# Optimization experiments

Hardware: AMD Instinct MI355X
Metric: run time of the kernel (lower is better)

Reference implementation:

```python
import jax, jax.numpy as jnp
import numpy as np

N, H, D, G = 8192, 512, 256, 64
TAU, LAM, ALPHA, BETA = 0.5, 0.5, 1.0, 1.0
EPS_G, EPS_L = 1e-6, 1e-5


def setup_inputs() -> dict:
    key = jax.random.key(0)
    ks = jax.random.split(key, 8)
    za = jax.random.normal(ks[0], (N, H), dtype=jnp.float32)
    zb = jax.random.normal(ks[1], (N, H), dtype=jnp.float32)
    pos = jax.random.uniform(ks[2], (N, N), dtype=jnp.float32)
    batch = (jnp.arange(N, dtype=jnp.int32) * G) // N  # sorted, covers all G groups
    s_h = np.sqrt(2.0 / H).astype(np.float32)  # kaiming fan_in relu
    W1 = jax.random.normal(ks[3], (H, H), dtype=jnp.float32) * s_h
    b1 = jnp.zeros((H,), dtype=jnp.float32)
    W2 = jax.random.normal(ks[4], (H, H), dtype=jnp.float32) * s_h
    b2 = jnp.zeros((H,), dtype=jnp.float32)
    W3 = jax.random.normal(ks[5], (H, D), dtype=jnp.float32) * s_h
    b3 = jnp.zeros((D,), dtype=jnp.float32)
    a1 = jnp.full((1,), 0.5, dtype=jnp.float32)
    g1 = jnp.ones((H,), dtype=jnp.float32)
    be1 = jnp.zeros((H,), dtype=jnp.float32)
    a2 = jnp.full((1,), 0.5, dtype=jnp.float32)
    g2 = jnp.ones((H,), dtype=jnp.float32)
    be2 = jnp.zeros((H,), dtype=jnp.float32)
    return {"za": za, "zb": zb, "pos": pos, "batch": batch,
            "W1": W1, "b1": b1, "a1": a1, "g1": g1, "be1": be1,
            "W2": W2, "b2": b2, "a2": a2, "g2": g2, "be2": be2,
            "W3": W3, "b3": b3}


def _project(z, W1, b1, a1, g1, be1, W2, b2, a2, g2, be2, W3, b3):
    h = z @ W1 + b1
    h = jnp.tanh(a1 * h) * g1 + be1  # DyT
    h = h @ W2 + b2
    h = jnp.tanh(a2 * h) * g2 + be2  # DyT
    p = h @ W3 + b3
    return p * jax.nn.sigmoid(p)  # z1_proj * sigmoid(z1_proj)


def reference(za, zb, pos, batch, W1, b1, a1, g1, be1, W2, b2, a2, g2, be2, W3, b3):
    za_p = _project(za, W1, b1, a1, g1, be1, W2, b2, a2, g2, be2, W3, b3)
    zb_p = _project(zb, W1, b1, a1, g1, be1, W2, b2, a2, g2, be2, W3, b3)

    # exp(cosine / tau): same matrix used by global_contrast (sim) and local_contrast
    na = jnp.linalg.norm(za_p, axis=-1, keepdims=True)  # [N,1]
    nb = jnp.linalg.norm(zb_p, axis=-1, keepdims=True)  # [N,1]
    m = jnp.exp((za_p @ zb_p.T) / (na * nb.T) / TAU)    # [N,N]

    # global contrast
    a2b = m / (jnp.sum(m, axis=1, keepdims=True) + EPS_G)
    lori_a = -jnp.mean(jnp.log(jnp.sum(a2b * pos, axis=-1)))
    b2a = m.T
    b2a = b2a / (jnp.sum(b2a, axis=1, keepdims=True) + EPS_G)
    lori_b = -jnp.mean(jnp.log(jnp.sum(b2a * pos, axis=-1)))
    global_loss = LAM * lori_a + (1.0 - LAM) * lori_b

    # local contrast: per-group sums via one-hot matmul (replaces O(G^2) mask loop)
    pos_sim = jnp.diagonal(m)                              # [N]
    pos_sim_graph = jax.ops.segment_sum(pos_sim, batch, num_segments=G)  # [G]
    hot = jax.nn.one_hot(batch, G, dtype=m.dtype)          # [N,G]
    batch_sim = hot.T @ m @ hot                            # [G,G]
    graph_sim = jnp.diagonal(batch_sim)
    neg0 = jnp.sum(batch_sim, axis=0) - graph_sim
    neg1 = jnp.sum(batch_sim, axis=1) - graph_sim
    loss0 = jnp.mean(jnp.log(pos_sim_graph / (neg0 + EPS_L)))
    loss1 = jnp.mean(jnp.log(pos_sim_graph / (neg1 + EPS_L)))
    inter_loss = (loss0 + loss1) / 2.0
    inner_loss = -jnp.mean(jnp.log(pos_sim_graph / (graph_sim - pos_sim_graph + EPS_L)))
    local_loss = ALPHA * inter_loss + BETA * inner_loss

    total_loss = global_loss + local_loss
    return total_loss, jnp.concatenate((za_p, zb_p), axis=1)
```

## Files before the change

kernel.cpp:

```cpp
#include <hip/hip_runtime.h>
#include <hip/hip_bf16.h>
#include <cstdint>
#include <cstddef>


typedef __bf16 bf16;
typedef __bf16 bf16x4 __attribute__((ext_vector_type(4)));
typedef __bf16 bf16x8 __attribute__((ext_vector_type(8)));
typedef float  f32x4  __attribute__((ext_vector_type(4)));

#define NROWS 8192
#define HDIM  512
#define DDIM  256
#define GGRP  64
#define INV_TAU 2.0f

__device__ __forceinline__ void async_ld16(const void* g, void* l) {
    __builtin_amdgcn_global_load_lds(
        (__attribute__((address_space(1))) void*)(g),
        (__attribute__((address_space(3))) void*)(l), 16, 0, 0);
}

__device__ __forceinline__ void mfma_tile_128(
    const bf16* __restrict__ A, const bf16* __restrict__ Bt, int K,
    int row0, int col0, bf16* ldsA, bf16* ldsB, f32x4 acc[4][4])
{
    const int tid  = threadIdx.x;
    const int lane = tid & 63;
    const int wave = tid >> 6;
    const int wrow = (wave >> 1) * 64;
    const int wcol = (wave & 1) * 64;
    const int lrow = lane & 15;
    const int lk8  = (lane >> 4) * 8;

#pragma unroll
    for (int i = 0; i < 4; i++)
#pragma unroll
        for (int j = 0; j < 4; j++) acc[i][j] = (f32x4){0.f, 0.f, 0.f, 0.f};

    for (int k0 = 0; k0 < K; k0 += 32) {
#pragma unroll
        for (int t = 0; t < 2; t++) {
            int f = t * 256 + tid;
            int r = f >> 2;
            int c = (f & 3) * 8;
            async_ld16(A  + (size_t)(row0 + r) * K + k0 + c,
                       ldsA + (size_t)(t * 256 + wave * 64) * 8);
            async_ld16(Bt + (size_t)(col0 + r) * K + k0 + c,
                       ldsB + (size_t)(t * 256 + wave * 64) * 8);
        }
        __syncthreads();

        bf16x8 af[4], bfr[4];
#pragma unroll
        for (int fi = 0; fi < 4; fi++)
            af[fi] = *(const bf16x8*)(ldsA + (wrow + fi * 16 + lrow) * 32 + lk8);
#pragma unroll
        for (int fj = 0; fj < 4; fj++)
            bfr[fj] = *(const bf16x8*)(ldsB + (wcol + fj * 16 + lrow) * 32 + lk8);
#pragma unroll
        for (int fi = 0; fi < 4; fi++)
#pragma unroll
            for (int fj = 0; fj < 4; fj++)
                acc[fi][fj] = __builtin_amdgcn_mfma_f32_16x16x32_bf16(
                    af[fi], bfr[fj], acc[fi][fj], 0, 0, 0);
        __syncthreads();
    }
}

__global__ __launch_bounds__(256) void gemm_dyt(
    const bf16* __restrict__ A, const bf16* __restrict__ Bt, bf16* __restrict__ C,
    int K, int N,
    const float* __restrict__ bias, const float* __restrict__ alph,
    const float* __restrict__ gam, const float* __restrict__ bet)
{
    __shared__ __align__(16) bf16 ldsA[128 * 32];
    __shared__ __align__(16) bf16 ldsB[128 * 32];
    f32x4 acc[4][4];
    const int row0 = blockIdx.y * 128, col0 = blockIdx.x * 128;
    mfma_tile_128(A, Bt, K, row0, col0, ldsA, ldsB, acc);

    const int lane = threadIdx.x & 63, wave = threadIdx.x >> 6;
    const int wrow = (wave >> 1) * 64, wcol = (wave & 1) * 64;
    const int lcol = lane & 15, lrg = (lane >> 4) * 4;
    const float a = alph[0];
#pragma unroll
    for (int fi = 0; fi < 4; fi++) {
        const int rbase = row0 + wrow + fi * 16 + lrg;
#pragma unroll
        for (int fj = 0; fj < 4; fj++) {
            const int cg = col0 + wcol + fj * 16 + lcol;
            const float bcol = bias[cg], gcol = gam[cg], becol = bet[cg];
#pragma unroll
            for (int r = 0; r < 4; r++) {
                float x = acc[fi][fj][r] + bcol;
                float y = tanhf(a * x) * gcol + becol;
                C[(size_t)(rbase + r) * N + cg] = (bf16)y;
            }
        }
    }
}

__global__ __launch_bounds__(256) void gemm_silu(
    const bf16* __restrict__ A, const bf16* __restrict__ Bt,
    bf16* __restrict__ P16, float* __restrict__ out1, float* __restrict__ n2,
    const float* __restrict__ bias)
{
    __shared__ __align__(16) bf16 ldsA[128 * 32];
    __shared__ __align__(16) bf16 ldsB[128 * 32];
    f32x4 acc[4][4];
    const int row0 = blockIdx.y * 128, col0 = blockIdx.x * 128;
    mfma_tile_128(A, Bt, 512, row0, col0, ldsA, ldsB, acc);

    const int lane = threadIdx.x & 63, wave = threadIdx.x >> 6;
    const int wrow = (wave >> 1) * 64, wcol = (wave & 1) * 64;
    const int lcol = lane & 15, lrg = (lane >> 4) * 4;

    float nacc[4][4];
#pragma unroll
    for (int i = 0; i < 4; i++)
#pragma unroll
        for (int r = 0; r < 4; r++) nacc[i][r] = 0.f;

#pragma unroll
    for (int fi = 0; fi < 4; fi++) {
        const int rbase = row0 + wrow + fi * 16 + lrg;
#pragma unroll
        for (int fj = 0; fj < 4; fj++) {
            const int cg = col0 + wcol + fj * 16 + lcol;
            const float bcol = bias[cg];
#pragma unroll
            for (int r = 0; r < 4; r++) {
                const int rg = rbase + r;
                float x = acc[fi][fj][r] + bcol;
                float y = x / (1.f + __expf(-x));
                P16[(size_t)rg * 256 + cg] = (bf16)y;
                size_t oidx = (rg < NROWS) ? ((size_t)rg * 512 + cg)
                                           : ((size_t)(rg - NROWS) * 512 + 256 + cg);
                out1[oidx] = y;
                nacc[fi][r] += y * y;
            }
        }
    }
#pragma unroll
    for (int fi = 0; fi < 4; fi++)
#pragma unroll
        for (int r = 0; r < 4; r++) {
            float v = nacc[fi][r];
            v += __shfl_xor(v, 1); v += __shfl_xor(v, 2);
            v += __shfl_xor(v, 4); v += __shfl_xor(v, 8);
            if (lcol == 0)
                atomicAdd(&n2[row0 + wrow + fi * 16 + lrg + r], v);
        }
}

template <int PASS1>
__global__ __launch_bounds__(256) void sim_kernel(
    const bf16* __restrict__ PA, const bf16* __restrict__ PB,
    const float* __restrict__ rnA, const float* __restrict__ rnB,
    const float* __restrict__ pos,
    float* __restrict__ rsum, float* __restrict__ wsum,
    float* __restrict__ bsim, float* __restrict__ psg)
{
    __shared__ __align__(16) bf16 ldsA[128 * 32];
    __shared__ __align__(16) bf16 ldsB[128 * 32];
    f32x4 acc[4][4];
    const int I = blockIdx.y, J = blockIdx.x;
    const int row0 = I * 128, col0 = J * 128;
    mfma_tile_128(PA, PB, 256, row0, col0, ldsA, ldsB, acc);

    const int lane = threadIdx.x & 63, wave = threadIdx.x >> 6;
    const int wrow = (wave >> 1) * 64, wcol = (wave & 1) * 64;
    const int lcol = lane & 15, lrg = (lane >> 4) * 4;

    float racc[4][4], sacc[4][4];
#pragma unroll
    for (int i = 0; i < 4; i++)
#pragma unroll
        for (int r = 0; r < 4; r++) { racc[i][r] = 0.f; sacc[i][r] = 0.f; }
    float msum = 0.f;

#pragma unroll
    for (int fi = 0; fi < 4; fi++) {
        const int rbase = row0 + wrow + fi * 16 + lrg;
        float rna[4];
#pragma unroll
        for (int r = 0; r < 4; r++) rna[r] = rnA[rbase + r] * INV_TAU;
#pragma unroll
        for (int fj = 0; fj < 4; fj++) {
            const int cg = col0 + wcol + fj * 16 + lcol;
            const float rnb = rnB[cg];
#pragma unroll
            for (int r = 0; r < 4; r++) {
                float mval = __expf(acc[fi][fj][r] * rna[r] * rnb);
                float pv = pos[(size_t)(rbase + r) * NROWS + cg];
                racc[fi][r] += mval;
                sacc[fi][r] += mval * pv;
                if (PASS1) {
                    msum += mval;
                    if (I == J && (rbase + r) == cg)
                        atomicAdd(&psg[I], mval);
                }
            }
        }
    }
#pragma unroll
    for (int fi = 0; fi < 4; fi++)
#pragma unroll
        for (int r = 0; r < 4; r++) {
            float rv = racc[fi][r], sv = sacc[fi][r];
            rv += __shfl_xor(rv, 1); rv += __shfl_xor(rv, 2);
            rv += __shfl_xor(rv, 4); rv += __shfl_xor(rv, 8);
            sv += __shfl_xor(sv, 1); sv += __shfl_xor(sv, 2);
            sv += __shfl_xor(sv, 4); sv += __shfl_xor(sv, 8);
            if (lcol == 0) {
                const int rg = row0 + wrow + fi * 16 + lrg + r;
                atomicAdd(&rsum[rg], rv);
                atomicAdd(&wsum[rg], sv);
            }
        }
    if (PASS1) {
        msum += __shfl_xor(msum, 1);  msum += __shfl_xor(msum, 2);
        msum += __shfl_xor(msum, 4);  msum += __shfl_xor(msum, 8);
        msum += __shfl_xor(msum, 16); msum += __shfl_xor(msum, 32);
        if (lane == 0) atomicAdd(&bsim[I * GGRP + J], msum);
    }
}

__global__ void cast4_kernel(const float4* __restrict__ x, bf16x4* __restrict__ y, int n4)
{
    int i = blockIdx.x * blockDim.x + threadIdx.x;
    if (i < n4) {
        float4 v = x[i];
        bf16x4 o;
        o[0] = (bf16)v.x; o[1] = (bf16)v.y; o[2] = (bf16)v.z; o[3] = (bf16)v.w;
        y[i] = o;
    }
}

__global__ void transpose_cast(const float* __restrict__ W, bf16* __restrict__ Wt,
                               int R, int C)
{
    __shared__ float tile[32][33];
    const int c0 = blockIdx.x * 32, r0 = blockIdx.y * 32;
    const int tx = threadIdx.x, ty = threadIdx.y;
    for (int i = ty; i < 32; i += 8)
        tile[i][tx] = W[(size_t)(r0 + i) * C + c0 + tx];
    __syncthreads();
    for (int i = ty; i < 32; i += 8)
        Wt[(size_t)(c0 + i) * R + r0 + tx] = (bf16)tile[tx][i];
}

__global__ void rsqrt_kernel(const float* __restrict__ x, float* __restrict__ y, int n)
{
    int i = blockIdx.x * blockDim.x + threadIdx.x;
    if (i < n) y[i] = rsqrtf(fmaxf(x[i], 1e-30f));
}

__global__ void loss_kernel(
    const float* __restrict__ rowsum, const float* __restrict__ colsum,
    const float* __restrict__ sa, const float* __restrict__ sb,
    const float* __restrict__ bs, const float* __restrict__ psg,
    float* __restrict__ out)
{
    __shared__ float red[8];
    const int tid = threadIdx.x;
    float la = 0.f, lb = 0.f;
    for (int i = tid; i < NROWS; i += 256) {
        la += __logf(sa[i] / (rowsum[i] + 1e-6f));
        lb += __logf(sb[i] / (colsum[i] + 1e-6f));
    }
    for (int m = 1; m < 64; m <<= 1) {
        la += __shfl_xor(la, m);
        lb += __shfl_xor(lb, m);
    }
    if ((tid & 63) == 0) { red[tid >> 6] = la; red[4 + (tid >> 6)] = lb; }
    __syncthreads();

    float l0 = 0.f, l1 = 0.f, lin = 0.f;
    if (tid < GGRP) {
        const float d = bs[tid * GGRP + tid];
        float c0 = 0.f, c1 = 0.f;
        for (int a = 0; a < GGRP; a++) { c0 += bs[a * GGRP + tid]; c1 += bs[tid * GGRP + a]; }
        const float p = psg[tid];
        l0  = __logf(p / (c0 - d + 1e-5f));
        l1  = __logf(p / (c1 - d + 1e-5f));
        lin = __logf(p / (d - p + 1e-5f));
    }
    for (int m = 1; m < 64; m <<= 1) {
        l0 += __shfl_xor(l0, m); l1 += __shfl_xor(l1, m); lin += __shfl_xor(lin, m);
    }
    if (tid == 0) {
        const float lat = red[0] + red[1] + red[2] + red[3];
        const float lbt = red[4] + red[5] + red[6] + red[7];
        const float lori_a = -lat / (float)NROWS;
        const float lori_b = -lbt / (float)NROWS;
        const float global_loss = 0.5f * (lori_a + lori_b);
        const float inter = 0.5f * (l0 + l1) / (float)GGRP;
        const float inner = -lin / (float)GGRP;
        out[0] = global_loss + inter + inner;
    }
}

extern "C" void kernel_launch(void* const* d_in, const int* in_sizes, int n_in,
                              void* d_out, int out_size, void* d_ws, size_t ws_size,
                              hipStream_t stream)
{
    const float* za  = (const float*)d_in[0];
    const float* zb  = (const float*)d_in[1];
    const float* pos = (const float*)d_in[2];
    const float* W1  = (const float*)d_in[4];
    const float* b1  = (const float*)d_in[5];
    const float* a1  = (const float*)d_in[6];
    const float* g1  = (const float*)d_in[7];
    const float* be1 = (const float*)d_in[8];
    const float* W2  = (const float*)d_in[9];
    const float* b2  = (const float*)d_in[10];
    const float* a2  = (const float*)d_in[11];
    const float* g2  = (const float*)d_in[12];
    const float* be2 = (const float*)d_in[13];
    const float* W3  = (const float*)d_in[14];
    const float* b3  = (const float*)d_in[15];
    float* out = (float*)d_out;

    char* ws = (char*)d_ws;
    float* rowsum = (float*)(ws);
    float* colsum = rowsum + 8192;
    float* s_a    = colsum + 8192;
    float* s_b    = s_a + 8192;
    float* n2     = s_b + 8192;
    float* bsim   = n2 + 16384;
    float* psg    = bsim + 4096;
    const size_t accum_bytes = (size_t)(8192 * 4 + 16384 + 4096 + 64) * 4;

    float* rn  = (float*)(ws + 213248);
    bf16* Z16  = (bf16*)(ws + 213248 + 65536);
    bf16* h1   = Z16 + (size_t)16384 * 512;
    bf16* p16  = h1 + (size_t)16384 * 512;
    bf16* W1t  = p16 + (size_t)16384 * 256;
    bf16* W2t  = W1t + (size_t)512 * 512;
    bf16* W3t  = W2t + (size_t)512 * 512;

    hipMemsetAsync(d_ws, 0, accum_bytes, stream);

    const int n4 = NROWS * HDIM / 4;
    cast4_kernel<<<n4 / 256, 256, 0, stream>>>((const float4*)za, (bf16x4*)Z16, n4);
    cast4_kernel<<<n4 / 256, 256, 0, stream>>>((const float4*)zb,
                                               (bf16x4*)(Z16 + (size_t)NROWS * HDIM), n4);
    dim3 tb(32, 8);
    transpose_cast<<<dim3(16, 16), tb, 0, stream>>>(W1, W1t, 512, 512);
    transpose_cast<<<dim3(16, 16), tb, 0, stream>>>(W2, W2t, 512, 512);
    transpose_cast<<<dim3(8, 16),  tb, 0, stream>>>(W3, W3t, 512, 256);

    gemm_dyt<<<dim3(4, 128), 256, 0, stream>>>(Z16, W1t, h1, 512, 512, b1, a1, g1, be1);
    gemm_dyt<<<dim3(4, 128), 256, 0, stream>>>(h1, W2t, Z16 , 512, 512, b2, a2, g2, be2);
    gemm_silu<<<dim3(2, 128), 256, 0, stream>>>(Z16, W3t, p16, out + 1, n2, b3);
    rsqrt_kernel<<<16384 / 256, 256, 0, stream>>>(n2, rn, 16384);

    const bf16* pa = p16;
    const bf16* pb = p16 + (size_t)NROWS * DDIM;
    sim_kernel<1><<<dim3(64, 64), 256, 0, stream>>>(pa, pb, rn, rn + NROWS, pos,
                                                    rowsum, s_a, bsim, psg);
    sim_kernel<0><<<dim3(64, 64), 256, 0, stream>>>(pb, pa, rn + NROWS, rn, pos,
                                                    colsum, s_b, nullptr, nullptr);

    loss_kernel<<<1, 256, 0, stream>>>(rowsum, colsum, s_a, s_b, bsim, psg, out);
}
```

Before: 825.0 us.

## Fuse both similarity passes into one kernel sharing the pos tile

Merges the two sim_kernel launches into a single 512-thread kernel. Each half of the block computes one direction (A·Bᵀ or B·Aᵀ) for the same tile, and both halves reuse one register-prefetched pos tile, so the large pos matrix is read from memory once instead of twice. The pos load is issued before the MFMA loop so it can overlap with the GEMM. The single-block loss reduction is split into a parallel row-loss kernel plus a small final kernel. GEMM load address arithmetic is also hoisted out of the k-loop. The 64-float pos buffer per thread raises register pressure and could cause spills or lower occupancy.

```diff
diff --git a/kernel.cpp b/kernel.cpp
--- a/kernel.cpp
+++ b/kernel.cpp
@@ -23,9 +23,8 @@
 
 __device__ __forceinline__ void mfma_tile_128(
     const bf16* __restrict__ A, const bf16* __restrict__ Bt, int K,
-    int row0, int col0, bf16* ldsA, bf16* ldsB, f32x4 acc[4][4])
-{
-    const int tid  = threadIdx.x;
+    int row0, int col0, bf16* ldsA, bf16* ldsB, f32x4 acc[4][4], int tid)
+{
     const int lane = tid & 63;
     const int wave = tid >> 6;
     const int wrow = (wave >> 1) * 64;
@@ -33,22 +32,26 @@
     const int lrow = lane & 15;
     const int lk8  = (lane >> 4) * 8;
 
+    const int sr = tid >> 2;
+    const int sc = (tid & 3) * 8;
+    const bf16* gA0 = A  + (size_t)(row0 + sr) * K + sc;
+    const bf16* gA1 = gA0 + (size_t)64 * K;
+    const bf16* gB0 = Bt + (size_t)(col0 + sr) * K + sc;
+    const bf16* gB1 = gB0 + (size_t)64 * K;
+    bf16* dA0 = ldsA + (wave * 64) * 8;
+    bf16* dA1 = ldsA + (256 + wave * 64) * 8;
+    bf16* dB0 = ldsB + (wave * 64) * 8;
+    bf16* dB1 = ldsB + (256 + wave * 64) * 8;
+
 #pragma unroll
     for (int i = 0; i < 4; i++)
 #pragma unroll
         for (int j = 0; j < 4; j++) acc[i][j] = (f32x4){0.f, 0.f, 0.f, 0.f};
 
     for (int k0 = 0; k0 < K; k0 += 32) {
-#pragma unroll
-        for (int t = 0; t < 2; t++) {
-            int f = t * 256 + tid;
-            int r = f >> 2;
-            int c = (f & 3) * 8;
-            async_ld16(A  + (size_t)(row0 + r) * K + k0 + c,
-                       ldsA + (size_t)(t * 256 + wave * 64) * 8);
-            async_ld16(Bt + (size_t)(col0 + r) * K + k0 + c,
-                       ldsB + (size_t)(t * 256 + wave * 64) * 8);
-        }
+        async_ld16(gA0, dA0); async_ld16(gA1, dA1);
+        async_ld16(gB0, dB0); async_ld16(gB1, dB1);
+        gA0 += 32; gA1 += 32; gB0 += 32; gB1 += 32;
         __syncthreads();
 
         bf16x8 af[4], bfr[4];
@@ -78,7 +81,7 @@
     __shared__ __align__(16) bf16 ldsB[128 * 32];
     f32x4 acc[4][4];
     const int row0 = blockIdx.y * 128, col0 = blockIdx.x * 128;
-    mfma_tile_128(A, Bt, K, row0, col0, ldsA, ldsB, acc);
+    mfma_tile_128(A, Bt, K, row0, col0, ldsA, ldsB, acc, threadIdx.x);
 
     const int lane = threadIdx.x & 63, wave = threadIdx.x >> 6;
     const int wrow = (wave >> 1) * 64, wcol = (wave & 1) * 64;
@@ -110,7 +113,7 @@
     __shared__ __align__(16) bf16 ldsB[128 * 32];
     f32x4 acc[4][4];
     const int row0 = blockIdx.y * 128, col0 = blockIdx.x * 128;
-    mfma_tile_128(A, Bt, 512, row0, col0, ldsA, ldsB, acc);
+    mfma_tile_128(A, Bt, 512, row0, col0, ldsA, ldsB, acc, threadIdx.x);
 
     const int lane = threadIdx.x & 63, wave = threadIdx.x >> 6;
     const int wrow = (wave >> 1) * 64, wcol = (wave & 1) * 64;
@@ -154,24 +157,45 @@
         }
 }
 
-template <int PASS1>
-__global__ __launch_bounds__(256) void sim_kernel(
+__global__ __launch_bounds__(512, 2) void sim_fused(
     const bf16* __restrict__ PA, const bf16* __restrict__ PB,
     const float* __restrict__ rnA, const float* __restrict__ rnB,
     const float* __restrict__ pos,
-    float* __restrict__ rsum, float* __restrict__ wsum,
+    float* __restrict__ rowsum, float* __restrict__ colsum,
+    float* __restrict__ s_a, float* __restrict__ s_b,
     float* __restrict__ bsim, float* __restrict__ psg)
 {
-    __shared__ __align__(16) bf16 ldsA[128 * 32];
-    __shared__ __align__(16) bf16 ldsB[128 * 32];
-    f32x4 acc[4][4];
+    __shared__ __align__(16) bf16 lds[2][2][128 * 32];
+    const int half = threadIdx.x >> 8;
+    const int tid  = threadIdx.x & 255;
     const int I = blockIdx.y, J = blockIdx.x;
     const int row0 = I * 128, col0 = J * 128;
-    mfma_tile_128(PA, PB, 256, row0, col0, ldsA, ldsB, acc);
-
-    const int lane = threadIdx.x & 63, wave = threadIdx.x >> 6;
+
+    const bf16* Aop = half ? PB : PA;
+    const bf16* Bop = half ? PA : PB;
+    const float* rnR = half ? rnB : rnA;
+    const float* rnC = half ? rnA : rnB;
+    float* outR = half ? colsum : rowsum;
+    float* outS = half ? s_b : s_a;
+
+    const int lane = tid & 63, wave = tid >> 6;
     const int wrow = (wave >> 1) * 64, wcol = (wave & 1) * 64;
     const int lcol = lane & 15, lrg = (lane >> 4) * 4;
+
+    float pv[4][4][4];
+#pragma unroll
+    for (int fi = 0; fi < 4; fi++)
+#pragma unroll
+        for (int r = 0; r < 4; r++) {
+            const float* prow = pos + (size_t)(row0 + wrow + fi * 16 + lrg + r) * NROWS
+                                    + col0 + wcol + lcol;
+#pragma unroll
+            for (int fj = 0; fj < 4; fj++) pv[fi][fj][r] = prow[fj * 16];
+        }
+
+    f32x4 acc[4][4];
+    mfma_tile_128(Aop, Bop, 256, row0, col0,
+                  (bf16*)lds[half][0], (bf16*)lds[half][1], acc, tid);
 
     float racc[4][4], sacc[4][4];
 #pragma unroll
@@ -185,18 +209,17 @@
         const int rbase = row0 + wrow + fi * 16 + lrg;
         float rna[4];
 #pragma unroll
-        for (int r = 0; r < 4; r++) rna[r] = rnA[rbase + r] * INV_TAU;
+        for (int r = 0; r < 4; r++) rna[r] = rnR[rbase + r] * INV_TAU;
 #pragma unroll
         for (int fj = 0; fj < 4; fj++) {
             const int cg = col0 + wcol + fj * 16 + lcol;
-            const float rnb = rnB[cg];
+            const float rnc = rnC[cg];
 #pragma unroll
             for (int r = 0; r < 4; r++) {
-                float mval = __expf(acc[fi][fj][r] * rna[r] * rnb);
-                float pv = pos[(size_t)(rbase + r) * NROWS + cg];
+                float mval = __expf(acc[fi][fj][r] * rna[r] * rnc);
                 racc[fi][r] += mval;
-                sacc[fi][r] += mval * pv;
-                if (PASS1) {
+                sacc[fi][r] += mval * pv[fi][fj][r];
+                if (half == 0) {
                     msum += mval;
                     if (I == J && (rbase + r) == cg)
                         atomicAdd(&psg[I], mval);
@@ -215,11 +238,11 @@
             sv += __shfl_xor(sv, 4); sv += __shfl_xor(sv, 8);
             if (lcol == 0) {
                 const int rg = row0 + wrow + fi * 16 + lrg + r;
-                atomicAdd(&rsum[rg], rv);
-                atomicAdd(&wsum[rg], sv);
+                atomicAdd(&outR[rg], rv);
+                atomicAdd(&outS[rg], sv);
             }
         }
-    if (PASS1) {
+    if (half == 0) {
         msum += __shfl_xor(msum, 1);  msum += __shfl_xor(msum, 2);
         msum += __shfl_xor(msum, 4);  msum += __shfl_xor(msum, 8);
         msum += __shfl_xor(msum, 16); msum += __shfl_xor(msum, 32);
@@ -257,44 +280,41 @@
     if (i < n) y[i] = rsqrtf(fmaxf(x[i], 1e-30f));
 }
 
-__global__ void loss_kernel(
-    const float* __restrict__ rowsum, const float* __restrict__ colsum,
-    const float* __restrict__ sa, const float* __restrict__ sb,
+__global__ __launch_bounds__(256) void loss_rows(
+    const float* __restrict__ sa, const float* __restrict__ rowsum,
+    const float* __restrict__ sb, const float* __restrict__ colsum,
+    float* __restrict__ gsum)
+{
+    __shared__ float red[8];
+    const int i = blockIdx.x * 256 + threadIdx.x;
+    float la = __logf(sa[i] / (rowsum[i] + 1e-6f));
+    float lb = __logf(sb[i] / (colsum[i] + 1e-6f));
+    for (int m = 1; m < 64; m <<= 1) { la += __shfl_xor(la, m); lb += __shfl_xor(lb, m); }
+    const int w = threadIdx.x >> 6;
+    if ((threadIdx.x & 63) == 0) { red[w] = la; red[4 + w] = lb; }
+    __syncthreads();
+    if (threadIdx.x == 0)  atomicAdd(&gsum[0], red[0] + red[1] + red[2] + red[3]);
+    if (threadIdx.x == 64) atomicAdd(&gsum[1], red[4] + red[5] + red[6] + red[7]);
+}
+
+__global__ void loss_final(
     const float* __restrict__ bs, const float* __restrict__ psg,
-    float* __restrict__ out)
-{
-    __shared__ float red[8];
-    const int tid = threadIdx.x;
-    float la = 0.f, lb = 0.f;
-    for (int i = tid; i < NROWS; i += 256) {
-        la += __logf(sa[i] / (rowsum[i] + 1e-6f));
-        lb += __logf(sb[i] / (colsum[i] + 1e-6f));
-    }
-    for (int m = 1; m < 64; m <<= 1) {
-        la += __shfl_xor(la, m);
-        lb += __shfl_xor(lb, m);
-    }
-    if ((tid & 63) == 0) { red[tid >> 6] = la; red[4 + (tid >> 6)] = lb; }
-    __syncthreads();
-
-    float l0 = 0.f, l1 = 0.f, lin = 0.f;
-    if (tid < GGRP) {
-        const float d = bs[tid * GGRP + tid];
-        float c0 = 0.f, c1 = 0.f;
-        for (int a = 0; a < GGRP; a++) { c0 += bs[a * GGRP + tid]; c1 += bs[tid * GGRP + a]; }
-        const float p = psg[tid];
-        l0  = __logf(p / (c0 - d + 1e-5f));
-        l1  = __logf(p / (c1 - d + 1e-5f));
-        lin = __logf(p / (d - p + 1e-5f));
-    }
+    const float* __restrict__ gsum, float* __restrict__ out)
+{
+    const int t = threadIdx.x;
+    float c0 = 0.f, c1 = 0.f;
+    for (int a = 0; a < GGRP; a++) { c0 += bs[a * GGRP + t]; c1 += bs[t * GGRP + a]; }
+    const float d = bs[t * (GGRP + 1)];
+    const float p = psg[t];
+    float l0  = __logf(p / (c0 - d + 1e-5f));
+    float l1  = __logf(p / (c1 - d + 1e-5f));
+    float lin = __logf(p / (d - p + 1e-5f));
     for (int m = 1; m < 64; m <<= 1) {
         l0 += __shfl_xor(l0, m); l1 += __shfl_xor(l1, m); lin += __shfl_xor(lin, m);
     }
-    if (tid == 0) {
-        const float lat = red[0] + red[1] + red[2] + red[3];
-        const float lbt = red[4] + red[5] + red[6] + red[7];
-        const float lori_a = -lat / (float)NROWS;
-        const float lori_b = -lbt / (float)NROWS;
+    if (t == 0) {
+        const float lori_a = -gsum[0] / (float)NROWS;
+        const float lori_b = -gsum[1] / (float)NROWS;
         const float global_loss = 0.5f * (lori_a + lori_b);
         const float inter = 0.5f * (l0 + l1) / (float)GGRP;
         const float inner = -lin / (float)GGRP;
@@ -331,10 +351,11 @@
     float* n2     = s_b + 8192;
     float* bsim   = n2 + 16384;
     float* psg    = bsim + 4096;
-    const size_t accum_bytes = (size_t)(8192 * 4 + 16384 + 4096 + 64) * 4;
-
-    float* rn  = (float*)(ws + 213248);
-    bf16* Z16  = (bf16*)(ws + 213248 + 65536);
+    float* gsum   = psg + 64;
+    const size_t accum_bytes = (size_t)(8192 * 4 + 16384 + 4096 + 64 + 2) * 4;
+
+    float* rn  = (float*)(ws + 213504);
+    bf16* Z16  = (bf16*)(ws + 213504 + 65536);
     bf16* h1   = Z16 + (size_t)16384 * 512;
     bf16* p16  = h1 + (size_t)16384 * 512;
     bf16* W1t  = p16 + (size_t)16384 * 256;
@@ -359,10 +380,9 @@
 
     const bf16* pa = p16;
     const bf16* pb = p16 + (size_t)NROWS * DDIM;
-    sim_kernel<1><<<dim3(64, 64), 256, 0, stream>>>(pa, pb, rn, rn + NROWS, pos,
-                                                    rowsum, s_a, bsim, psg);
-    sim_kernel<0><<<dim3(64, 64), 256, 0, stream>>>(pb, pa, rn + NROWS, rn, pos,
-                                                    colsum, s_b, nullptr, nullptr);
-
-    loss_kernel<<<1, 256, 0, stream>>>(rowsum, colsum, s_a, s_b, bsim, psg, out);
-}
+    sim_fused<<<dim3(64, 64), 512, 0, stream>>>(pa, pb, rn, rn + NROWS, pos,
+                                                rowsum, colsum, s_a, s_b, bsim, psg);
+
+    loss_rows<<<32, 256, 0, stream>>>(s_a, rowsum, s_b, colsum, gsum);
+    loss_final<<<1, 64, 0, stream>>>(bsim, psg, gsum, out);
+}
```

New measurement: 904.3 us. 1.1x slower.
